# Optimization experiments

Hardware: AMD Instinct MI355X
Metric: run time of the kernel (lower is better)

The kernel has to match this reference:

```python
import jax, jax.numpy as jnp
import numpy as np


def masked_softmax(x, m, axis):
    # x clamped, multiplicatively masked before and after exp (faithful to source)
    x = jnp.clip(x, -15.0, 15.0)
    x = x * m
    e_x = jnp.exp(x - jnp.max(x, axis=axis, keepdims=True))
    e_x = e_x * m
    return e_x / (jnp.sum(e_x, axis=axis, keepdims=True) + 1e-6)


def setup_inputs() -> dict:
    key = jax.random.key(0)
    kC, kQ, kcm, kqm, kwC, kwQ, kwm = jax.random.split(key, 7)
    B, Lc, Lq, d = 16, 1024, 256, 512
    C = jax.random.normal(kC, (B, Lc, d), dtype=jnp.float32)
    Q = jax.random.normal(kQ, (B, Lq, d), dtype=jnp.float32)
    Cmask = jax.random.randint(kcm, (B, Lc), 0, 2, dtype=jnp.int32)
    Qmask = jax.random.randint(kqm, (B, Lq), 0, 2, dtype=jnp.int32)
    # xavier_uniform bound for shape (d, 1): sqrt(6/(d+1))
    bnd = float(np.sqrt(6.0 / (d + 1)))
    w4C = jax.random.uniform(kwC, (d, 1), jnp.float32, -bnd, bnd)
    w4Q = jax.random.uniform(kwQ, (d, 1), jnp.float32, -bnd, bnd)
    bnd_m = float(np.sqrt(6.0 / (1 + d)))
    w4mlu = jax.random.uniform(kwm, (1, 1, d), jnp.float32, -bnd_m, bnd_m)
    bias = jnp.zeros((1,), dtype=jnp.float32)
    return {"C": C, "Q": Q, "Cmask": Cmask, "Qmask": Qmask,
            "w4C": w4C, "w4Q": w4Q, "w4mlu": w4mlu, "bias": bias}


def reference(C, Q, Cmask, Qmask, w4C, w4Q, w4mlu, bias):
    # trilinear similarity S: [B, Lc, Lq]
    sub0 = jnp.matmul(C, w4C)                      # [B, Lc, 1]
    sub1 = jnp.swapaxes(jnp.matmul(Q, w4Q), 1, 2)  # [B, 1, Lq]
    sub2 = jnp.matmul(C * w4mlu, jnp.swapaxes(Q, 1, 2))  # [B, Lc, Lq]
    S = sub0 + sub1 + sub2 + bias

    Cm = Cmask.astype(jnp.float32)[:, :, None]  # [B, Lc, 1]
    Qm = Qmask.astype(jnp.float32)[:, None, :]  # [B, 1, Lq]
    S1 = masked_softmax(S, Qm, axis=2)  # rows over question
    S2 = masked_softmax(S, Cm, axis=1)  # cols over context

    A = jnp.matmul(S1, Q)                                   # [B, Lc, d]
    Bt = jnp.matmul(jnp.matmul(S1, jnp.swapaxes(S2, 1, 2)), C)  # [B, Lc, d]
    return jnp.concatenate([C, A, C * A, C * Bt], axis=2)   # [B, Lc, 4d]
```

## Files before the change

### kernel.cpp

```cpp
#include <hip/hip_runtime.h>
#include <cstdint>
#include <cstddef>


typedef __attribute__((ext_vector_type(8))) short short8;
typedef __attribute__((ext_vector_type(4))) short short4v;
typedef __attribute__((ext_vector_type(4))) float f32x4;
typedef __attribute__((ext_vector_type(8))) __bf16 bf16x8;

__device__ __forceinline__ short f2bf(float f) {
  unsigned u = __builtin_bit_cast(unsigned, f);
  u += 0x7fffu + ((u >> 16) & 1u);
  return (short)(u >> 16);
}

__device__ __forceinline__ void gload16(const void* g, void* l) {
  __builtin_amdgcn_global_load_lds(
      (const __attribute__((address_space(1))) void*)g,
      (__attribute__((address_space(3))) void*)l, 16, 0, 0);
}

__device__ __forceinline__ f32x4 mfma16(short8 a, short8 b, f32x4 c) {
  return __builtin_amdgcn_mfma_f32_16x16x32_bf16(
      __builtin_bit_cast(bf16x8, a), __builtin_bit_cast(bf16x8, b), c, 0, 0, 0);
}

__device__ __forceinline__ short8 pack8(float4 x, float4 y) {
  short8 s;
  s[0] = f2bf(x.x); s[1] = f2bf(x.y); s[2] = f2bf(x.z); s[3] = f2bf(x.w);
  s[4] = f2bf(y.x); s[5] = f2bf(y.y); s[6] = f2bf(y.z); s[7] = f2bf(y.w);
  return s;
}
__device__ __forceinline__ float dot4(float4 a, float4 b) {
  return a.x * b.x + a.y * b.y + a.z * b.z + a.w * b.w;
}


__device__ __forceinline__ void gemm_core(const short* __restrict__ A,
                                          const short* __restrict__ B, int K,
                                          int lda, int ldb, int m0, int n0,
                                          short* ldsA, short* ldsB,
                                          f32x4 (&acc)[4][4]) {
  const int tid = threadIdx.x;
  const int lane = tid & 63;
  const int wave = tid >> 6;
  const int wr = (wave >> 1) * 64, wc = (wave & 1) * 64;
  const int fr = lane & 15;
  const int fk = (lane >> 4) * 8;
  const int srow = tid >> 2;
  const int skoff = (tid & 3) * 8;

  const short* Ag = A + (size_t)(m0 + srow) * lda + skoff;
  const short* Ag2 = A + (size_t)(m0 + 64 + srow) * lda + skoff;
  const short* Bg = B + (size_t)(n0 + srow) * ldb + skoff;
  const short* Bg2 = B + (size_t)(n0 + 64 + srow) * ldb + skoff;
  short* la = ldsA + tid * 8;
  short* la2 = ldsA + 64 * 32 + tid * 8;
  short* lb = ldsB + tid * 8;
  short* lb2 = ldsB + 64 * 32 + tid * 8;

  for (int k0 = 0; k0 < K; k0 += 32) {
    gload16(Ag + k0, la);
    gload16(Ag2 + k0, la2);
    gload16(Bg + k0, lb);
    gload16(Bg2 + k0, lb2);
    __syncthreads();
    short8 af[4], bf[4];
#pragma unroll
    for (int m = 0; m < 4; ++m)
      af[m] = *(const short8*)(ldsA + (wr + m * 16 + fr) * 32 + fk);
#pragma unroll
    for (int n = 0; n < 4; ++n)
      bf[n] = *(const short8*)(ldsB + (wc + n * 16 + fr) * 32 + fk);
#pragma unroll
    for (int m = 0; m < 4; ++m)
#pragma unroll
      for (int n = 0; n < 4; ++n) acc[m][n] = mfma16(af[m], bf[n], acc[m][n]);
    __syncthreads();
  }
}

__device__ __forceinline__ void gemm_core64(const short* __restrict__ A,
                                            const short* __restrict__ B, int K,
                                            int lda, int ldb, int m0, int n0,
                                            short* ldsA, short* ldsB,
                                            f32x4 (&acc)[2][2]) {
  const int tid = threadIdx.x;
  const int lane = tid & 63;
  const int wave = tid >> 6;
  const int wr = (wave >> 1) * 32, wc = (wave & 1) * 32;
  const int fr = lane & 15;
  const int fk = (lane >> 4) * 8;
  const int srow = tid >> 2;
  const int skoff = (tid & 3) * 8;

  const short* Ag = A + (size_t)(m0 + srow) * lda + skoff;
  const short* Bg = B + (size_t)(n0 + srow) * ldb + skoff;
  short* la = ldsA + tid * 8;
  short* lb = ldsB + tid * 8;

  for (int k0 = 0; k0 < K; k0 += 32) {
    gload16(Ag + k0, la);
    gload16(Bg + k0, lb);
    __syncthreads();
    short8 af[2], bf[2];
#pragma unroll
    for (int m = 0; m < 2; ++m)
      af[m] = *(const short8*)(ldsA + (wr + m * 16 + fr) * 32 + fk);
#pragma unroll
    for (int n = 0; n < 2; ++n)
      bf[n] = *(const short8*)(ldsB + (wc + n * 16 + fr) * 32 + fk);
#pragma unroll
    for (int m = 0; m < 2; ++m)
#pragma unroll
      for (int n = 0; n < 2; ++n) acc[m][n] = mfma16(af[m], bf[n], acc[m][n]);
    __syncthreads();
  }
}


__device__ __forceinline__ void prep_tile64(const float* __restrict__ ip,
                                            short* __restrict__ op, int outld,
                                            int r0, int c0, short* tile) {
  const int tx = threadIdx.x & 15, ty = threadIdx.x >> 4;
#pragma unroll
  for (int i = 0; i < 64; i += 16) {
    float4 v = *(const float4*)(ip + (size_t)(r0 + ty + i) * 512 + c0 + tx * 4);
    short* t = tile + (ty + i) * 66 + tx * 4;
    t[0] = f2bf(v.x); t[1] = f2bf(v.y); t[2] = f2bf(v.z); t[3] = f2bf(v.w);
  }
  __syncthreads();
#pragma unroll
  for (int i = 0; i < 64; i += 16) {
    const int orow = ty + i, ocol = tx * 4;
    short4v o;
#pragma unroll
    for (int j = 0; j < 4; ++j) o[j] = tile[(ocol + j) * 66 + orow];
    *(short4v*)(op + (size_t)(c0 + orow) * outld + r0 + ocol) = o;
  }
}


__device__ __forceinline__ void s_fused_body(
    const float* __restrict__ C, const float* __restrict__ Q,
    const int* __restrict__ Qmask, const int* __restrict__ Cmask,
    const float* __restrict__ w4C, const float* __restrict__ w4Q,
    const float* __restrict__ w4mlu, const float* __restrict__ bias,
    short* __restrict__ S1, short* __restrict__ Eu,
    float* __restrict__ partial, int b, int mblk, char* sm) {
  short* ldsA = (short*)sm;
  short* ldsB = (short*)(sm + 64 * 32 * 2);
  short* eT = (short*)sm;
  float* sub0_l = (float*)(sm + 36864);
  float* sub1_l = (float*)(sm + 37120);
  float(*redS)[64] = (float(*)[64])(sm + 38144);

  const int m0 = mblk * 64;
  const int tid = threadIdx.x;
  const int lane = tid & 63, wave = tid >> 6;

  const float* Cb = C + ((size_t)b * 1024 + m0) * 512;
  const float* Qb = Q + (size_t)b * 256 * 512;

  const int srow = tid >> 2;
  const int skk = (tid & 3) * 8;

  f32x4 acc[4][4];
  {
    f32x4 z = {0.f, 0.f, 0.f, 0.f};
#pragma unroll
    for (int m = 0; m < 4; ++m)
#pragma unroll
      for (int n = 0; n < 4; ++n) acc[m][n] = z;
  }
  float dotA = 0.f;
  float dotB[4] = {0.f, 0.f, 0.f, 0.f};

  const int fr = lane & 15, fk = (lane >> 4) * 8;

  for (int k0 = 0; k0 < 512; k0 += 32) {
    float4 a0 = *(const float4*)(Cb + (size_t)srow * 512 + k0 + skk);
    float4 a1 = *(const float4*)(Cb + (size_t)srow * 512 + k0 + skk + 4);
    float4 q0[4], q1[4];
#pragma unroll
    for (int r4 = 0; r4 < 4; ++r4) {
      const float* qp = Qb + (size_t)(srow + 64 * r4) * 512 + k0 + skk;
      q0[r4] = *(const float4*)qp;
      q1[r4] = *(const float4*)(qp + 4);
    }
    float4 wm0 = *(const float4*)(w4mlu + k0 + skk);
    float4 wm1 = *(const float4*)(w4mlu + k0 + skk + 4);
    float4 wc0 = *(const float4*)(w4C + k0 + skk);
    float4 wc1 = *(const float4*)(w4C + k0 + skk + 4);
    float4 wq0 = *(const float4*)(w4Q + k0 + skk);
    float4 wq1 = *(const float4*)(w4Q + k0 + skk + 4);

    dotA += dot4(a0, wc0) + dot4(a1, wc1);
#pragma unroll
    for (int r4 = 0; r4 < 4; ++r4)
      dotB[r4] += dot4(q0[r4], wq0) + dot4(q1[r4], wq1);

    float4 am0, am1;
    am0.x = a0.x * wm0.x; am0.y = a0.y * wm0.y;
    am0.z = a0.z * wm0.z; am0.w = a0.w * wm0.w;
    am1.x = a1.x * wm1.x; am1.y = a1.y * wm1.y;
    am1.z = a1.z * wm1.z; am1.w = a1.w * wm1.w;
    short8 as = pack8(am0, am1);
    short8 bs[4];
#pragma unroll
    for (int r4 = 0; r4 < 4; ++r4) bs[r4] = pack8(q0[r4], q1[r4]);

    __syncthreads();
    *(short8*)(ldsA + srow * 32 + skk) = as;
#pragma unroll
    for (int r4 = 0; r4 < 4; ++r4)
      *(short8*)(ldsB + (srow + 64 * r4) * 32 + skk) = bs[r4];
    __syncthreads();

    short8 af[4], bfv[4];
#pragma unroll
    for (int m = 0; m < 4; ++m)
      af[m] = *(const short8*)(ldsA + (m * 16 + fr) * 32 + fk);
#pragma unroll
    for (int n = 0; n < 4; ++n)
      bfv[n] = *(const short8*)(ldsB + (wave * 64 + n * 16 + fr) * 32 + fk);
#pragma unroll
    for (int m = 0; m < 4; ++m)
#pragma unroll
      for (int n = 0; n < 4; ++n) acc[m][n] = mfma16(af[m], bfv[n], acc[m][n]);
  }

  dotA += __shfl_xor(dotA, 1, 64);
  dotA += __shfl_xor(dotA, 2, 64);
#pragma unroll
  for (int r4 = 0; r4 < 4; ++r4) {
    dotB[r4] += __shfl_xor(dotB[r4], 1, 64);
    dotB[r4] += __shfl_xor(dotB[r4], 2, 64);
  }
  if ((tid & 3) == 0) {
    sub0_l[srow] = dotA;
#pragma unroll
    for (int r4 = 0; r4 < 4; ++r4) sub1_l[srow + 64 * r4] = dotB[r4];
  }
  __syncthreads();

  const float bv = bias[0];
  const int cc = lane & 15, cr = (lane >> 4) * 4;
  float qmv[4];
#pragma unroll
  for (int n = 0; n < 4; ++n)
    qmv[n] = (float)Qmask[b * 256 + wave * 64 + n * 16 + cc];
  float cmv[4][4];
#pragma unroll
  for (int m = 0; m < 4; ++m)
#pragma unroll
    for (int i = 0; i < 4; ++i)
      cmv[m][i] = (float)Cmask[b * 1024 + m0 + m * 16 + cr + i];

#pragma unroll
  for (int m = 0; m < 4; ++m)
#pragma unroll
    for (int n = 0; n < 4; ++n)
#pragma unroll
      for (int i = 0; i < 4; ++i) {
        float v = acc[m][n][i] + sub0_l[m * 16 + cr + i] +
                  sub1_l[wave * 64 + n * 16 + cc] + bv;
        acc[m][n][i] = fminf(15.f, fmaxf(-15.f, v));
      }

  float ps[4] = {0.f, 0.f, 0.f, 0.f};
#pragma unroll
  for (int m = 0; m < 4; ++m)
#pragma unroll
    for (int n = 0; n < 4; ++n) {
      short4v o;
#pragma unroll
      for (int i = 0; i < 4; ++i) {
        float cm = cmv[m][i];
        float ec = cm * __expf(acc[m][n][i] * cm - 8.f);
        ps[n] += ec;
        o[i] = f2bf(ec);
      }
      *(short4v*)(eT + (wave * 64 + n * 16 + cc) * 72 + m * 16 + cr) = o;
    }
#pragma unroll
  for (int n = 0; n < 4; ++n) {
    ps[n] += __shfl_xor(ps[n], 16, 64);
    ps[n] += __shfl_xor(ps[n], 32, 64);
  }
  if (lane < 16) {
#pragma unroll
    for (int n = 0; n < 4; ++n)
      partial[((size_t)b * 16 + mblk) * 256 + wave * 64 + n * 16 + cc] = ps[n];
  }
  __syncthreads();

  short* Eub = Eu + (size_t)b * 262144 + m0;
#pragma unroll
  for (int it = 0; it < 8; ++it) {
    int q = it * 32 + wave * 8 + (lane >> 3);
    int k = lane & 7;
    short8 v = *(const short8*)(eT + q * 72 + k * 8);
    *(short8*)(Eub + (size_t)q * 1024 + k * 8) = v;
  }

  float rs[4][4];
#pragma unroll
  for (int m = 0; m < 4; ++m)
#pragma unroll
    for (int i = 0; i < 4; ++i) {
      rs[m][i] = 0.f;
#pragma unroll
      for (int n = 0; n < 4; ++n) {
        float eq = qmv[n] * __expf(acc[m][n][i] * qmv[n] - 8.f);
        acc[m][n][i] = eq;
        rs[m][i] += eq;
      }
    }
#pragma unroll
  for (int m = 0; m < 4; ++m)
#pragma unroll
    for (int i = 0; i < 4; ++i) {
      rs[m][i] += __shfl_xor(rs[m][i], 1, 64);
      rs[m][i] += __shfl_xor(rs[m][i], 2, 64);
      rs[m][i] += __shfl_xor(rs[m][i], 4, 64);
      rs[m][i] += __shfl_xor(rs[m][i], 8, 64);
    }
  if (cc == 0) {
#pragma unroll
    for (int m = 0; m < 4; ++m)
#pragma unroll
      for (int i = 0; i < 4; ++i) redS[wave][m * 16 + cr + i] = rs[m][i];
  }
  __syncthreads();

  short* S1b = S1 + (size_t)b * 262144 + (size_t)m0 * 256;
#pragma unroll
  for (int m = 0; m < 4; ++m)
#pragma unroll
    for (int i = 0; i < 4; ++i) {
      int r = m * 16 + cr + i;
      float sum = redS[0][r] + redS[1][r] + redS[2][r] + redS[3][r];
      float inv = 1.f / (sum + 1e-6f);
#pragma unroll
      for (int n = 0; n < 4; ++n)
        S1b[(size_t)r * 256 + wave * 64 + n * 16 + cc] =
            f2bf(acc[m][n][i] * inv);
    }
}


__global__ __launch_bounds__(256) void stage1(
    const float* __restrict__ C, const float* __restrict__ Q,
    const int* __restrict__ Qmask, const int* __restrict__ Cmask,
    const float* __restrict__ w4C, const float* __restrict__ w4Q,
    const float* __restrict__ w4mlu, const float* __restrict__ bias,
    short* __restrict__ S1, short* __restrict__ Eu,
    float* __restrict__ partial, short* __restrict__ Ctb,
    short* __restrict__ QT) {
  __shared__ __attribute__((aligned(16))) char sm[39168];
  const int id = blockIdx.x;
  if (id < 256) {
    s_fused_body(C, Q, Qmask, Cmask, w4C, w4Q, w4mlu, bias, S1, Eu, partial,
                 id >> 4, id & 15, sm);
  } else if (id < 2304) {
    const int p = id - 256, b = p >> 7, t = p & 127;
    prep_tile64(C + (size_t)b * 1024 * 512, Ctb + (size_t)b * 512 * 1024, 1024,
                (t >> 3) * 64, (t & 7) * 64, (short*)sm);
  } else {
    const int p = id - 2304, b = p >> 5, t = p & 31;
    prep_tile64(Q + (size_t)b * 256 * 512, QT + (size_t)b * 1024 * 256, 256,
                (t >> 3) * 64, (t & 7) * 64, (short*)sm);
  }
}


__global__ __launch_bounds__(256) void stage2(
    const short* __restrict__ Ctb, const short* __restrict__ Eu,
    const float* __restrict__ partial, short* __restrict__ QT,
    const short* __restrict__ S1, const float* __restrict__ C,
    float* __restrict__ out) {
  __shared__ __attribute__((aligned(16))) char sm[16384];
  short* ldsA = (short*)sm;
  short* ldsB = (short*)(sm + 8192);
  const int id = blockIdx.x;
  const int lane = threadIdx.x & 63, wave = threadIdx.x >> 6;
  const int cr = (lane >> 4) * 4, cc = lane & 15;

  if (id < 512) {
    const int b = id >> 5, r = id & 31;
    const int m0 = (r >> 2) * 128, n0 = (r & 3) * 128;
    const int wr = (wave >> 1) * 64, wc = (wave & 1) * 64;
    f32x4 acc[4][4];
    {
      f32x4 z = {0.f, 0.f, 0.f, 0.f};
#pragma unroll
      for (int m = 0; m < 4; ++m)
#pragma unroll
        for (int n = 0; n < 4; ++n) acc[m][n] = z;
    }
    gemm_core(S1 + (size_t)b * 1024 * 256, QT + (size_t)b * 1024 * 256, 256,
              256, 256, m0, n0, ldsA, ldsB, acc);
#pragma unroll
    for (int m = 0; m < 4; ++m)
#pragma unroll
      for (int n = 0; n < 4; ++n)
#pragma unroll
        for (int i = 0; i < 4; ++i) {
          int rr = m0 + wr + m * 16 + cr + i;
          int c = n0 + wc + n * 16 + cc;
          float a = acc[m][n][i];
          float cv = C[((size_t)b * 1024 + rr) * 512 + c];
          size_t base = ((size_t)b * 1024 + rr) * 2048;
          __builtin_nontemporal_store(cv, &out[base + c]);
          __builtin_nontemporal_store(a, &out[base + 512 + c]);
          __builtin_nontemporal_store(cv * a, &out[base + 1024 + c]);
        }
  } else {
    const int t = id - 512, b = t >> 5, r = t & 31;
    const int m0 = (r >> 2) * 64, n0 = (r & 3) * 64;
    const int wr = (wave >> 1) * 32, wc = (wave & 1) * 32;
    f32x4 acc[2][2];
    {
      f32x4 z = {0.f, 0.f, 0.f, 0.f};
#pragma unroll
      for (int m = 0; m < 2; ++m)
#pragma unroll
        for (int n = 0; n < 2; ++n) acc[m][n] = z;
    }
    gemm_core64(Ctb + (size_t)b * 512 * 1024, Eu + (size_t)b * 256 * 1024,
                1024, 1024, 1024, m0, n0, ldsA, ldsB, acc);
    const float* pb = partial + (size_t)b * 16 * 256;
    float invv[2];
#pragma unroll
    for (int n = 0; n < 2; ++n) {
      int c = n0 + wc + n * 16 + cc;
      float s = 0.f;
#pragma unroll
      for (int k = 0; k < 16; ++k) s += pb[k * 256 + c];
      invv[n] = 1.f / (s + 1e-6f);
    }
    short* Tp = QT + (size_t)b * 1024 * 256 + 512 * 256;
#pragma unroll
    for (int m = 0; m < 2; ++m)
#pragma unroll
      for (int n = 0; n < 2; ++n)
#pragma unroll
        for (int i = 0; i < 4; ++i) {
          int rr = m0 + wr + m * 16 + cr + i;
          int c = n0 + wc + n * 16 + cc;
          Tp[(size_t)rr * 256 + c] = f2bf(acc[m][n][i] * invv[n]);
        }
  }
}


__global__ __launch_bounds__(256) void gemm_ABbot(const short* __restrict__ S1,
                                                  const short* __restrict__ QT,
                                                  const float* __restrict__ C,
                                                  float* __restrict__ out) {
  __shared__ __attribute__((aligned(16))) short ldsA[128 * 32];
  __shared__ __attribute__((aligned(16))) short ldsB[128 * 32];
  const int b = blockIdx.z;
  const int m0 = blockIdx.x * 128, n0 = 512 + blockIdx.y * 128;
  f32x4 acc[4][4];
  {
    f32x4 z = {0.f, 0.f, 0.f, 0.f};
#pragma unroll
    for (int m = 0; m < 4; ++m)
#pragma unroll
      for (int n = 0; n < 4; ++n) acc[m][n] = z;
  }
  const int lane = threadIdx.x & 63, wave = threadIdx.x >> 6;
  const int wr = (wave >> 1) * 64, wc = (wave & 1) * 64;
  const int cr = (lane >> 4) * 4, cc = lane & 15;
  gemm_core(S1 + (size_t)b * 1024 * 256, QT + (size_t)b * 1024 * 256, 256, 256,
            256, m0, n0, ldsA, ldsB, acc);
#pragma unroll
  for (int m = 0; m < 4; ++m)
#pragma unroll
    for (int n = 0; n < 4; ++n)
#pragma unroll
      for (int i = 0; i < 4; ++i) {
        int rr = m0 + wr + m * 16 + cr + i;
        int cq = (n0 - 512) + wc + n * 16 + cc;
        float cv = C[((size_t)b * 1024 + rr) * 512 + cq];
        size_t base = ((size_t)b * 1024 + rr) * 2048;
        __builtin_nontemporal_store(cv * acc[m][n][i], &out[base + 1536 + cq]);
      }
}


extern "C" void kernel_launch(void* const* d_in, const int* in_sizes, int n_in,
                              void* d_out, int out_size, void* d_ws,
                              size_t ws_size, hipStream_t stream) {
  const float* C = (const float*)d_in[0];
  const float* Q = (const float*)d_in[1];
  const int* Cmask = (const int*)d_in[2];
  const int* Qmask = (const int*)d_in[3];
  const float* w4C = (const float*)d_in[4];
  const float* w4Q = (const float*)d_in[5];
  const float* w4mlu = (const float*)d_in[6];
  const float* bias = (const float*)d_in[7];
  float* out = (float*)d_out;

  size_t off = 0;
  auto alloc = [&](size_t n) {
    void* p = (char*)d_ws + off;
    off += (n + 255) & ~(size_t)255;
    return p;
  };
  short* Ctb = (short*)alloc((size_t)16 * 512 * 1024 * 2);
  short* QT = (short*)alloc((size_t)16 * 1024 * 256 * 2);
  short* S1 = (short*)alloc((size_t)16 * 1024 * 256 * 2);
  short* Eu = (short*)alloc((size_t)16 * 256 * 1024 * 2);
  float* partial = (float*)alloc((size_t)16 * 16 * 256 * 4);

  stage1<<<dim3(2816), dim3(256), 0, stream>>>(C, Q, Qmask, Cmask, w4C, w4Q,
                                               w4mlu, bias, S1, Eu, partial,
                                               Ctb, QT);
  stage2<<<dim3(1024), dim3(256), 0, stream>>>(Ctb, Eu, partial, QT, S1, C,
                                               out);
  gemm_ABbot<<<dim3(8, 4, 16), dim3(256), 0, stream>>>(S1, QT, C, out);
}
```

Before: 105.5 us.

## Regroup stages: copy C passthrough in prep, merge A and Bt GEMMs

```diff
diff --git a/kernel.cpp b/kernel.cpp
--- a/kernel.cpp
+++ b/kernel.cpp
@@ -119,9 +119,34 @@
 }
 
 
-__device__ __forceinline__ void prep_tile64(const float* __restrict__ ip,
-                                            short* __restrict__ op, int outld,
-                                            int r0, int c0, short* tile) {
+__device__ __forceinline__ void prep_tile64_c(const float* __restrict__ ip,
+                                              short* __restrict__ op,
+                                              float* __restrict__ outp,
+                                              int r0, int c0, short* tile) {
+  const int tx = threadIdx.x & 15, ty = threadIdx.x >> 4;
+#pragma unroll
+  for (int i = 0; i < 64; i += 16) {
+    float4 v = *(const float4*)(ip + (size_t)(r0 + ty + i) * 512 + c0 + tx * 4);
+    f32x4 vv = {v.x, v.y, v.z, v.w};
+    __builtin_nontemporal_store(
+        vv, (f32x4*)(outp + (size_t)(r0 + ty + i) * 2048 + c0 + tx * 4));
+    short* t = tile + (ty + i) * 66 + tx * 4;
+    t[0] = f2bf(v.x); t[1] = f2bf(v.y); t[2] = f2bf(v.z); t[3] = f2bf(v.w);
+  }
+  __syncthreads();
+#pragma unroll
+  for (int i = 0; i < 64; i += 16) {
+    const int orow = ty + i, ocol = tx * 4;
+    short4v o;
+#pragma unroll
+    for (int j = 0; j < 4; ++j) o[j] = tile[(ocol + j) * 66 + orow];
+    *(short4v*)(op + (size_t)(c0 + orow) * 1024 + r0 + ocol) = o;
+  }
+}
+
+__device__ __forceinline__ void prep_tile64_q(const float* __restrict__ ip,
+                                              short* __restrict__ op,
+                                              int r0, int c0, short* tile) {
   const int tx = threadIdx.x & 15, ty = threadIdx.x >> 4;
 #pragma unroll
   for (int i = 0; i < 64; i += 16) {
@@ -136,7 +161,7 @@
     short4v o;
 #pragma unroll
     for (int j = 0; j < 4; ++j) o[j] = tile[(ocol + j) * 66 + orow];
-    *(short4v*)(op + (size_t)(c0 + orow) * outld + r0 + ocol) = o;
+    *(short4v*)(op + (size_t)(c0 + orow) * 256 + r0 + ocol) = o;
   }
 }
 
@@ -357,7 +382,7 @@
     const float* __restrict__ w4mlu, const float* __restrict__ bias,
     short* __restrict__ S1, short* __restrict__ Eu,
     float* __restrict__ partial, short* __restrict__ Ctb,
-    short* __restrict__ QT) {
+    short* __restrict__ QT, float* __restrict__ out) {
   __shared__ __attribute__((aligned(16))) char sm[39168];
   const int id = blockIdx.x;
   if (id < 256) {
@@ -365,42 +390,88 @@
                  id >> 4, id & 15, sm);
   } else if (id < 2304) {
     const int p = id - 256, b = p >> 7, t = p & 127;
-    prep_tile64(C + (size_t)b * 1024 * 512, Ctb + (size_t)b * 512 * 1024, 1024,
-                (t >> 3) * 64, (t & 7) * 64, (short*)sm);
+    prep_tile64_c(C + (size_t)b * 1024 * 512, Ctb + (size_t)b * 512 * 1024,
+                  out + (size_t)b * 1024 * 2048, (t >> 3) * 64, (t & 7) * 64,
+                  (short*)sm);
   } else {
     const int p = id - 2304, b = p >> 5, t = p & 31;
-    prep_tile64(Q + (size_t)b * 256 * 512, QT + (size_t)b * 1024 * 256, 256,
-                (t >> 3) * 64, (t & 7) * 64, (short*)sm);
-  }
-}
-
-
-__global__ __launch_bounds__(256) void stage2(
+    prep_tile64_q(Q + (size_t)b * 256 * 512, QT + (size_t)b * 1024 * 256,
+                  (t >> 3) * 64, (t & 7) * 64, (short*)sm);
+  }
+}
+
+
+__global__ __launch_bounds__(256) void gemm_T2s(
     const short* __restrict__ Ctb, const short* __restrict__ Eu,
-    const float* __restrict__ partial, short* __restrict__ QT,
-    const short* __restrict__ S1, const float* __restrict__ C,
-    float* __restrict__ out) {
-  __shared__ __attribute__((aligned(16))) char sm[16384];
-  short* ldsA = (short*)sm;
-  short* ldsB = (short*)(sm + 8192);
+    const float* __restrict__ partial, short* __restrict__ QT) {
+  __shared__ __attribute__((aligned(16))) short ldsA[64 * 32];
+  __shared__ __attribute__((aligned(16))) short ldsB[64 * 32];
   const int id = blockIdx.x;
+  const int b = id >> 5, r = id & 31;
+  const int m0 = (r >> 2) * 64, n0 = (r & 3) * 64;
   const int lane = threadIdx.x & 63, wave = threadIdx.x >> 6;
+  const int wr = (wave >> 1) * 32, wc = (wave & 1) * 32;
   const int cr = (lane >> 4) * 4, cc = lane & 15;
-
-  if (id < 512) {
-    const int b = id >> 5, r = id & 31;
-    const int m0 = (r >> 2) * 128, n0 = (r & 3) * 128;
-    const int wr = (wave >> 1) * 64, wc = (wave & 1) * 64;
-    f32x4 acc[4][4];
-    {
-      f32x4 z = {0.f, 0.f, 0.f, 0.f};
-#pragma unroll
-      for (int m = 0; m < 4; ++m)
-#pragma unroll
-        for (int n = 0; n < 4; ++n) acc[m][n] = z;
-    }
-    gemm_core(S1 + (size_t)b * 1024 * 256, QT + (size_t)b * 1024 * 256, 256,
-              256, 256, m0, n0, ldsA, ldsB, acc);
+  f32x4 acc[2][2];
+  {
+    f32x4 z = {0.f, 0.f, 0.f, 0.f};
+#pragma unroll
+    for (int m = 0; m < 2; ++m)
+#pragma unroll
+      for (int n = 0; n < 2; ++n) acc[m][n] = z;
+  }
+  gemm_core64(Ctb + (size_t)b * 512 * 1024, Eu + (size_t)b * 256 * 1024, 1024,
+              1024, 1024, m0, n0, ldsA, ldsB, acc);
+  const float* pb = partial + (size_t)b * 16 * 256;
+  float invv[2];
+#pragma unroll
+  for (int n = 0; n < 2; ++n) {
+    int c = n0 + wc + n * 16 + cc;
+    float s = 0.f;
+#pragma unroll
+    for (int k = 0; k < 16; ++k) s += pb[k * 256 + c];
+    invv[n] = 1.f / (s + 1e-6f);
+  }
+  short* Tp = QT + (size_t)b * 1024 * 256 + 512 * 256;
+#pragma unroll
+  for (int m = 0; m < 2; ++m)
+#pragma unroll
+    for (int n = 0; n < 2; ++n)
+#pragma unroll
+      for (int i = 0; i < 4; ++i) {
+        int rr = m0 + wr + m * 16 + cr + i;
+        int c = n0 + wc + n * 16 + cc;
+        Tp[(size_t)rr * 256 + c] = f2bf(acc[m][n][i] * invv[n]);
+      }
+}
+
+
+__global__ __launch_bounds__(256) void stage3(const short* __restrict__ S1,
+                                              const short* __restrict__ QT,
+                                              const float* __restrict__ C,
+                                              float* __restrict__ out) {
+  __shared__ __attribute__((aligned(16))) short ldsA[128 * 32];
+  __shared__ __attribute__((aligned(16))) short ldsB[128 * 32];
+  const int id = blockIdx.x;
+  const bool top = id < 512;
+  const int t = top ? id : id - 512;
+  const int b = t >> 5, r = t & 31;
+  const int m0 = (r >> 2) * 128;
+  const int n0 = (top ? 0 : 512) + (r & 3) * 128;
+  const int lane = threadIdx.x & 63, wave = threadIdx.x >> 6;
+  const int wr = (wave >> 1) * 64, wc = (wave & 1) * 64;
+  const int cr = (lane >> 4) * 4, cc = lane & 15;
+  f32x4 acc[4][4];
+  {
+    f32x4 z = {0.f, 0.f, 0.f, 0.f};
+#pragma unroll
+    for (int m = 0; m < 4; ++m)
+#pragma unroll
+      for (int n = 0; n < 4; ++n) acc[m][n] = z;
+  }
+  gemm_core(S1 + (size_t)b * 1024 * 256, QT + (size_t)b * 1024 * 256, 256, 256,
+            256, m0, n0, ldsA, ldsB, acc);
+  if (top) {
 #pragma unroll
     for (int m = 0; m < 4; ++m)
 #pragma unroll
@@ -412,82 +483,24 @@
           float a = acc[m][n][i];
           float cv = C[((size_t)b * 1024 + rr) * 512 + c];
           size_t base = ((size_t)b * 1024 + rr) * 2048;
-          __builtin_nontemporal_store(cv, &out[base + c]);
           __builtin_nontemporal_store(a, &out[base + 512 + c]);
           __builtin_nontemporal_store(cv * a, &out[base + 1024 + c]);
         }
   } else {
-    const int t = id - 512, b = t >> 5, r = t & 31;
-    const int m0 = (r >> 2) * 64, n0 = (r & 3) * 64;
-    const int wr = (wave >> 1) * 32, wc = (wave & 1) * 32;
-    f32x4 acc[2][2];
-    {
-      f32x4 z = {0.f, 0.f, 0.f, 0.f};
-#pragma unroll
-      for (int m = 0; m < 2; ++m)
-#pragma unroll
-        for (int n = 0; n < 2; ++n) acc[m][n] = z;
-    }
-    gemm_core64(Ctb + (size_t)b * 512 * 1024, Eu + (size_t)b * 256 * 1024,
-                1024, 1024, 1024, m0, n0, ldsA, ldsB, acc);
-    const float* pb = partial + (size_t)b * 16 * 256;
-    float invv[2];
-#pragma unroll
-    for (int n = 0; n < 2; ++n) {
-      int c = n0 + wc + n * 16 + cc;
-      float s = 0.f;
-#pragma unroll
-      for (int k = 0; k < 16; ++k) s += pb[k * 256 + c];
-      invv[n] = 1.f / (s + 1e-6f);
-    }
-    short* Tp = QT + (size_t)b * 1024 * 256 + 512 * 256;
-#pragma unroll
-    for (int m = 0; m < 2; ++m)
-#pragma unroll
-      for (int n = 0; n < 2; ++n)
+#pragma unroll
+    for (int m = 0; m < 4; ++m)
+#pragma unroll
+      for (int n = 0; n < 4; ++n)
 #pragma unroll
         for (int i = 0; i < 4; ++i) {
           int rr = m0 + wr + m * 16 + cr + i;
-          int c = n0 + wc + n * 16 + cc;
-          Tp[(size_t)rr * 256 + c] = f2bf(acc[m][n][i] * invv[n]);
+          int cq = (n0 - 512) + wc + n * 16 + cc;
+          float cv = C[((size_t)b * 1024 + rr) * 512 + cq];
+          size_t base = ((size_t)b * 1024 + rr) * 2048;
+          __builtin_nontemporal_store(cv * acc[m][n][i],
+                                      &out[base + 1536 + cq]);
         }
   }
-}
-
-
-__global__ __launch_bounds__(256) void gemm_ABbot(const short* __restrict__ S1,
-                                                  const short* __restrict__ QT,
-                                                  const float* __restrict__ C,
-                                                  float* __restrict__ out) {
-  __shared__ __attribute__((aligned(16))) short ldsA[128 * 32];
-  __shared__ __attribute__((aligned(16))) short ldsB[128 * 32];
-  const int b = blockIdx.z;
-  const int m0 = blockIdx.x * 128, n0 = 512 + blockIdx.y * 128;
-  f32x4 acc[4][4];
-  {
-    f32x4 z = {0.f, 0.f, 0.f, 0.f};
-#pragma unroll
-    for (int m = 0; m < 4; ++m)
-#pragma unroll
-      for (int n = 0; n < 4; ++n) acc[m][n] = z;
-  }
-  const int lane = threadIdx.x & 63, wave = threadIdx.x >> 6;
-  const int wr = (wave >> 1) * 64, wc = (wave & 1) * 64;
-  const int cr = (lane >> 4) * 4, cc = lane & 15;
-  gemm_core(S1 + (size_t)b * 1024 * 256, QT + (size_t)b * 1024 * 256, 256, 256,
-            256, m0, n0, ldsA, ldsB, acc);
-#pragma unroll
-  for (int m = 0; m < 4; ++m)
-#pragma unroll
-    for (int n = 0; n < 4; ++n)
-#pragma unroll
-      for (int i = 0; i < 4; ++i) {
-        int rr = m0 + wr + m * 16 + cr + i;
-        int cq = (n0 - 512) + wc + n * 16 + cc;
-        float cv = C[((size_t)b * 1024 + rr) * 512 + cq];
-        size_t base = ((size_t)b * 1024 + rr) * 2048;
-        __builtin_nontemporal_store(cv * acc[m][n][i], &out[base + 1536 + cq]);
-      }
 }
 
 
@@ -518,8 +531,7 @@
 
   stage1<<<dim3(2816), dim3(256), 0, stream>>>(C, Q, Qmask, Cmask, w4C, w4Q,
                                                w4mlu, bias, S1, Eu, partial,
-                                               Ctb, QT);
-  stage2<<<dim3(1024), dim3(256), 0, stream>>>(Ctb, Eu, partial, QT, S1, C,
-                                               out);
-  gemm_ABbot<<<dim3(8, 4, 16), dim3(256), 0, stream>>>(S1, QT, C, out);
-}
+                                               Ctb, QT, out);
+  gemm_T2s<<<dim3(512), dim3(256), 0, stream>>>(Ctb, Eu, partial, QT);
+  stage3<<<dim3(1024), dim3(256), 0, stream>>>(S1, QT, C, out);
+}
```

Result: no change. 107.6 us (+2.0%).
